# Performance work log

Measured on AMD Instinct MI355X. Metric: run time of the kernel, lower is better.

The kernel has to match this reference:

```python
import jax, jax.numpy as jnp
import numpy as np

NEG_INF = -1e9


def setup_inputs() -> dict:
    key = jax.random.key(0)
    ks = jax.random.split(key, 9)
    B, T, E, D, H = 64, 2048, 1024, 1024, 1024
    enc = jax.random.normal(ks[0], (B, T, E), dtype=jnp.float32)
    dec = jax.random.normal(ks[1], (B, D), dtype=jnp.float32)
    inp_mask = jax.random.randint(ks[2], (B, T), 0, 2, dtype=jnp.int32)
    s = 1.0 / np.sqrt(H)
    W_enc = jax.random.normal(ks[3], (E, H), dtype=jnp.float32) * s
    b_enc = jax.random.normal(ks[4], (H,), dtype=jnp.float32) * 0.01
    W_dec = jax.random.normal(ks[5], (D, H), dtype=jnp.float32) * s
    b_dec = jax.random.normal(ks[6], (H,), dtype=jnp.float32) * 0.01
    W_out = jax.random.normal(ks[7], (H, 1), dtype=jnp.float32) * s
    b_out = jax.random.normal(ks[8], (1,), dtype=jnp.float32) * 0.01
    return {"enc": enc, "dec": dec, "inp_mask": inp_mask,
            "W_enc": W_enc, "b_enc": b_enc, "W_dec": W_dec, "b_dec": b_dec,
            "W_out": W_out, "b_out": b_out}


def reference(enc, dec, inp_mask, W_enc, b_enc, W_dec, b_dec, W_out, b_out):
    # a: [B, T, H] = Linear(enc) + Linear(dec)[:, None, :]
    a = jnp.einsum('bte,eh->bth', enc, W_enc) + b_enc \
        + (dec @ W_dec + b_dec)[:, None, :]
    a = jnp.tanh(a)
    # scores: [B, T]
    scores = (jnp.einsum('bth,h->bt', a, W_out[:, 0]) + b_out[0])
    scores = jnp.where(inp_mask == 0, NEG_INF, scores)
    probs = jax.nn.softmax(scores, axis=1)            # [B, T]
    attn = jnp.einsum('bt,bte->be', probs, enc)       # [B, E]
    return (attn, probs)
```

## Files before the change

### kernel.cpp

```cpp
#include <hip/hip_runtime.h>
#include <hip/hip_bf16.h>

typedef __attribute__((ext_vector_type(4))) float f32x4;
typedef __attribute__((ext_vector_type(4))) unsigned int u32x4;

static constexpr int Bb = 64;
static constexpr int Tt = 2048;
static constexpr int Ee = 1024;
static constexpr int Hh = 1024;
static constexpr int ATTN_N = Bb * Ee;
static constexpr int PROB_N = Bb * Tt;

__device__ inline unsigned short f2bf(float f) {
    __hip_bfloat16 h = __float2bfloat16(f);
    return __builtin_bit_cast(unsigned short, h);
}

__device__ inline void gload_lds16(const unsigned short* g, unsigned short* l) {
    __builtin_amdgcn_global_load_lds(
        (const __attribute__((address_space(1))) void*)g,
        (__attribute__((address_space(3))) void*)l,
        16, 0, 0);
}

__global__ void wtrans_kernel(const float* __restrict__ w_enc,
                              unsigned short* __restrict__ w16t) {
    __shared__ float tile[32][33];
    const int bx = blockIdx.x & 31;
    const int by = blockIdx.x >> 5;
    const int tx = threadIdx.x & 31;
    const int ty = threadIdx.x >> 5;
#pragma unroll
    for (int j = 0; j < 4; ++j) {
        int e = by * 32 + ty + j * 8;
        int h = bx * 32 + tx;
        tile[ty + j * 8][tx] = w_enc[e * Hh + h];
    }
    __syncthreads();
#pragma unroll
    for (int j = 0; j < 4; ++j) {
        int h = bx * 32 + ty + j * 8;
        int e = by * 32 + tx;
        w16t[h * Ee + e] = f2bf(tile[tx][ty + j * 8]);
    }
}

__global__ void ddec_kernel(const float* __restrict__ dec,
                            const float* __restrict__ w_dec,
                            const float* __restrict__ b_dec,
                            const float* __restrict__ b_enc,
                            float* __restrict__ ddec) {
    const int b = blockIdx.y;
    const int h = blockIdx.x * 256 + threadIdx.x;
    float acc = b_dec[h] + b_enc[h];
    const float* dr = dec + b * Ee;
#pragma unroll 4
    for (int e = 0; e < Ee; ++e) {
        acc += dr[e] * w_dec[e * Hh + h];
    }
    ddec[b * Hh + h] = acc;
}

__global__ __launch_bounds__(512, 2) void gemm_score_kernel(
    const float* __restrict__ enc, const unsigned short* __restrict__ w16t,
    const float* __restrict__ ddec, const float* __restrict__ w_out,
    float* __restrict__ scores) {
    __shared__ unsigned short As[2][256 * 64];
    __shared__ unsigned short Bs[2][256 * 64];

    const int tid = threadIdx.x;
    const int lane = tid & 63;
    const int wid = tid >> 6;
    const int wm = wid >> 2;
    const int wn = wid & 3;
    const int lr = lane & 15;
    const int lg = lane >> 4;

    const int g = blockIdx.x;
    const int xcd = g & 7;
    const int slot = g >> 3;
    const int ntile = slot & 3;
    const int mtile = xcd * 64 + (slot >> 2);
    const int m0 = mtile * 256;
    const int n0 = ntile * 256;
    const int bidx = m0 >> 11;

    const int ar = tid >> 3;
    const int as = tid & 7;

    f32x4 aregs[8];

    auto loadA = [&](int kt) {
        const float* src = enc + (size_t)(m0 + ar) * Ee + kt * 64 + as * 8;
#pragma unroll
        for (int ci = 0; ci < 4; ++ci) {
            aregs[ci * 2]     = *reinterpret_cast<const f32x4*>(src + (size_t)(64 * ci) * Ee);
            aregs[ci * 2 + 1] = *reinterpret_cast<const f32x4*>(src + (size_t)(64 * ci) * Ee + 4);
        }
    };
    auto writeA = [&](int db) {
        char* abase = (char*)&As[db][0];
#pragma unroll
        for (int ci = 0; ci < 4; ++ci) {
            int r = ar + 64 * ci;
            u32x4 w;
            w.x = (unsigned)f2bf(aregs[2 * ci].x) | ((unsigned)f2bf(aregs[2 * ci].y) << 16);
            w.y = (unsigned)f2bf(aregs[2 * ci].z) | ((unsigned)f2bf(aregs[2 * ci].w) << 16);
            w.z = (unsigned)f2bf(aregs[2 * ci + 1].x) | ((unsigned)f2bf(aregs[2 * ci + 1].y) << 16);
            w.w = (unsigned)f2bf(aregs[2 * ci + 1].z) | ((unsigned)f2bf(aregs[2 * ci + 1].w) << 16);
            *reinterpret_cast<u32x4*>(abase + r * 128 + ((as * 16) ^ ((r & 7) << 4))) = w;
        }
    };
    auto stageB = [&](int kt, int db) {
        const int sg = (lane & 7) ^ (lane >> 3);
#pragma unroll
        for (int c = 0; c < 4; ++c) {
            int rr = (wid * 4 + c) * 8 + (lane >> 3);
            const unsigned short* src = w16t + (size_t)(n0 + rr) * Ee + kt * 64 + sg * 8;
            gload_lds16(src, &Bs[db][(wid * 4 + c) * 512]);
        }
    };

    f32x4 acc[8][4];
#pragma unroll
    for (int ni = 0; ni < 4; ++ni) {
        float dv = ddec[bidx * Hh + n0 + wn * 64 + ni * 16 + lr];
#pragma unroll
        for (int mi = 0; mi < 8; ++mi) {
            acc[mi][ni].x = dv; acc[mi][ni].y = dv;
            acc[mi][ni].z = dv; acc[mi][ni].w = dv;
        }
    }

    u32x4 af[4], bf[4];
    auto readB4 = [&](int db, int kh) {
        const char* bbase = (const char*)&Bs[db][0];
        const int kb = kh * 64 + lg * 16;
#pragma unroll
        for (int ni = 0; ni < 4; ++ni) {
            int r = wn * 64 + ni * 16 + lr;
            bf[ni] = *reinterpret_cast<const u32x4*>(bbase + r * 128 + (kb ^ ((r & 7) << 4)));
        }
    };
    auto readA4 = [&](int db, int kh, int mib) {
        const char* abase = (const char*)&As[db][0];
        const int kb = kh * 64 + lg * 16;
#pragma unroll
        for (int k = 0; k < 4; ++k) {
            int r = wm * 128 + (mib + k) * 16 + lr;
            af[k] = *reinterpret_cast<const u32x4*>(abase + r * 128 + (kb ^ ((r & 7) << 4)));
        }
    };
    auto mfma16 = [&](int mib) {
        __builtin_amdgcn_s_setprio(1);
#pragma unroll
        for (int k = 0; k < 4; ++k)
#pragma unroll
            for (int ni = 0; ni < 4; ++ni)
                asm("v_mfma_f32_16x16x32_bf16 %0, %1, %2, %0"
                    : "+v"(acc[mib + k][ni])
                    : "v"(af[k]), "v"(bf[ni]));
        __builtin_amdgcn_s_setprio(0);
    };

#define BARRIER() do { asm volatile("" ::: "memory"); \
    __builtin_amdgcn_s_barrier(); asm volatile("" ::: "memory"); } while (0)
#define LGKM0() asm volatile("s_waitcnt lgkmcnt(0)" ::: "memory")
#define VM0()   asm volatile("s_waitcnt vmcnt(0)" ::: "memory")

    loadA(0);
    stageB(0, 0);
    writeA(0);
    LGKM0();
    VM0();
    BARRIER();

#pragma unroll 1
    for (int t = 0; t < 16; ++t) {
        const int cur = t & 1;
        const bool stage = (t < 15);
        readB4(cur, 0);
        readA4(cur, 0, 0);
        if (stage) { stageB(t + 1, cur ^ 1); loadA(t + 1); }
        BARRIER(); LGKM0();
        mfma16(0);
        BARRIER();
        readA4(cur, 0, 4);
        BARRIER(); LGKM0();
        mfma16(4);
        BARRIER();
        readB4(cur, 1);
        readA4(cur, 1, 0);
        if (stage) writeA(cur ^ 1);
        BARRIER(); LGKM0();
        mfma16(0);
        BARRIER();
        readA4(cur, 1, 4);
        if (stage) VM0();
        BARRIER(); LGKM0();
        mfma16(4);
        BARRIER();
    }

    asm volatile("s_nop 7\n\ts_nop 7\n\ts_nop 7" ::: );

    float wout[4];
#pragma unroll
    for (int ni = 0; ni < 4; ++ni)
        wout[ni] = w_out[n0 + wn * 64 + ni * 16 + lr];

#pragma unroll
    for (int mi = 0; mi < 8; ++mi) {
#pragma unroll
        for (int i = 0; i < 4; ++i) {
            float s = 0.f;
#pragma unroll
            for (int ni = 0; ni < 4; ++ni) {
                float x = (i == 0) ? acc[mi][ni].x : (i == 1) ? acc[mi][ni].y
                           : (i == 2) ? acc[mi][ni].z : acc[mi][ni].w;
                float t = 1.f - 2.f / (__expf(2.f * x) + 1.f);
                s += t * wout[ni];
            }
            s += __shfl_xor(s, 1);
            s += __shfl_xor(s, 2);
            s += __shfl_xor(s, 4);
            s += __shfl_xor(s, 8);
            if (lr == 0) {
                int row = m0 + wm * 128 + mi * 16 + 4 * lg + i;
                atomicAdd(&scores[row], s);
            }
        }
    }
#undef BARRIER
#undef LGKM0
#undef VM0
}

__global__ __launch_bounds__(256) void softmax_kernel(float* __restrict__ sc,
                                                      const int* __restrict__ mask) {
    __shared__ float red[256];
    const int b = blockIdx.x;
    const int tid = threadIdx.x;
    float* row = sc + b * Tt;
    const int* mrow = mask + b * Tt;

    float v[8];
    float mx = -3.0e38f;
#pragma unroll
    for (int j = 0; j < 8; ++j) {
        int t = tid + j * 256;
        float s = row[t];
        v[j] = (mrow[t] == 0) ? -1.0e9f : s;
        mx = fmaxf(mx, v[j]);
    }
    red[tid] = mx;
    __syncthreads();
    for (int off = 128; off > 0; off >>= 1) {
        if (tid < off) red[tid] = fmaxf(red[tid], red[tid + off]);
        __syncthreads();
    }
    mx = red[0];
    __syncthreads();

    float p[8];
    float sum = 0.f;
#pragma unroll
    for (int j = 0; j < 8; ++j) {
        p[j] = __expf(v[j] - mx);
        sum += p[j];
    }
    red[tid] = sum;
    __syncthreads();
    for (int off = 128; off > 0; off >>= 1) {
        if (tid < off) red[tid] += red[tid + off];
        __syncthreads();
    }
    float inv = 1.f / red[0];
#pragma unroll
    for (int j = 0; j < 8; ++j)
        row[tid + j * 256] = p[j] * inv;
}

__global__ __launch_bounds__(256) void attn_kernel(const float* __restrict__ enc,
                                                   const float* __restrict__ probs,
                                                   float* __restrict__ attn) {
    __shared__ float pr[128];
    const int b = blockIdx.y;
    const int tc = blockIdx.x;
    const int tid = threadIdx.x;
    if (tid < 128) pr[tid] = probs[b * Tt + tc * 128 + tid];
    __syncthreads();

    const int e0 = tid * 4;
    f32x4 acc; acc.x = 0.f; acc.y = 0.f; acc.z = 0.f; acc.w = 0.f;
    const float* base = enc + (size_t)b * Tt * Ee + (size_t)tc * 128 * Ee + e0;
#pragma unroll 4
    for (int t = 0; t < 128; ++t) {
        f32x4 vv = *reinterpret_cast<const f32x4*>(base + (size_t)t * Ee);
        float pw = pr[t];
        acc.x += pw * vv.x; acc.y += pw * vv.y;
        acc.z += pw * vv.z; acc.w += pw * vv.w;
    }
    atomicAdd(&attn[b * Ee + e0 + 0], acc.x);
    atomicAdd(&attn[b * Ee + e0 + 1], acc.y);
    atomicAdd(&attn[b * Ee + e0 + 2], acc.z);
    atomicAdd(&attn[b * Ee + e0 + 3], acc.w);
}

extern "C" void kernel_launch(void* const* d_in, const int* in_sizes, int n_in,
                              void* d_out, int out_size, void* d_ws, size_t ws_size,
                              hipStream_t stream) {
    const float* enc      = (const float*)d_in[0];
    const float* dec      = (const float*)d_in[1];
    const int*   inp_mask = (const int*)d_in[2];
    const float* W_enc    = (const float*)d_in[3];
    const float* b_enc    = (const float*)d_in[4];
    const float* W_dec    = (const float*)d_in[5];
    const float* b_dec    = (const float*)d_in[6];
    const float* W_out    = (const float*)d_in[7];

    float* attn   = (float*)d_out;
    float* scores = (float*)d_out + ATTN_N;

    unsigned short* w16t = (unsigned short*)d_ws;
    float* ddec = attn;

    hipMemsetAsync(scores, 0, (size_t)PROB_N * sizeof(float), stream);

    wtrans_kernel<<<dim3(1024), 256, 0, stream>>>(W_enc, w16t);
    ddec_kernel<<<dim3(4, 64), 256, 0, stream>>>(dec, W_dec, b_dec, b_enc, ddec);
    gemm_score_kernel<<<dim3(2048), 512, 0, stream>>>(enc, w16t, ddec, W_out, scores);

    hipMemsetAsync(attn, 0, (size_t)ATTN_N * sizeof(float), stream);

    softmax_kernel<<<dim3(64), 256, 0, stream>>>(scores, inp_mask);
    attn_kernel<<<dim3(16, 64), 256, 0, stream>>>(enc, scores, attn);
}
```

Measured before the change: 665.4 us.

## Prefetch A tiles two k-steps ahead with double register buffers

The fp32 encoder A-tile global loads now go into two alternating register sets, so each load is issued two k-iterations before its LDS write instead of one. The main loop is unrolled by two so the register buffers can be swapped statically. Partial vmcnt waits replace the full drain, letting B staging finish while the next A loads stay in flight. This hides more global-memory latency at the cost of 32 extra VGPRs, which may reduce occupancy or cause spills.

```diff
diff --git a/kernel.cpp b/kernel.cpp
--- a/kernel.cpp
+++ b/kernel.cpp
@@ -88,26 +88,26 @@
     const int ar = tid >> 3;
     const int as = tid & 7;
 
-    f32x4 aregs[8];
-
-    auto loadA = [&](int kt) {
+    f32x4 rsA[8], rsB[8];
+
+    auto loadA = [&](int kt, f32x4 (&rs)[8]) {
         const float* src = enc + (size_t)(m0 + ar) * Ee + kt * 64 + as * 8;
 #pragma unroll
         for (int ci = 0; ci < 4; ++ci) {
-            aregs[ci * 2]     = *reinterpret_cast<const f32x4*>(src + (size_t)(64 * ci) * Ee);
-            aregs[ci * 2 + 1] = *reinterpret_cast<const f32x4*>(src + (size_t)(64 * ci) * Ee + 4);
-        }
-    };
-    auto writeA = [&](int db) {
+            rs[ci * 2]     = *reinterpret_cast<const f32x4*>(src + (size_t)(64 * ci) * Ee);
+            rs[ci * 2 + 1] = *reinterpret_cast<const f32x4*>(src + (size_t)(64 * ci) * Ee + 4);
+        }
+    };
+    auto writeA = [&](int db, f32x4 (&rs)[8]) {
         char* abase = (char*)&As[db][0];
 #pragma unroll
         for (int ci = 0; ci < 4; ++ci) {
             int r = ar + 64 * ci;
             u32x4 w;
-            w.x = (unsigned)f2bf(aregs[2 * ci].x) | ((unsigned)f2bf(aregs[2 * ci].y) << 16);
-            w.y = (unsigned)f2bf(aregs[2 * ci].z) | ((unsigned)f2bf(aregs[2 * ci].w) << 16);
-            w.z = (unsigned)f2bf(aregs[2 * ci + 1].x) | ((unsigned)f2bf(aregs[2 * ci + 1].y) << 16);
-            w.w = (unsigned)f2bf(aregs[2 * ci + 1].z) | ((unsigned)f2bf(aregs[2 * ci + 1].w) << 16);
+            w.x = (unsigned)f2bf(rs[2 * ci].x) | ((unsigned)f2bf(rs[2 * ci].y) << 16);
+            w.y = (unsigned)f2bf(rs[2 * ci].z) | ((unsigned)f2bf(rs[2 * ci].w) << 16);
+            w.z = (unsigned)f2bf(rs[2 * ci + 1].x) | ((unsigned)f2bf(rs[2 * ci + 1].y) << 16);
+            w.w = (unsigned)f2bf(rs[2 * ci + 1].z) | ((unsigned)f2bf(rs[2 * ci + 1].w) << 16);
             *reinterpret_cast<u32x4*>(abase + r * 128 + ((as * 16) ^ ((r & 7) << 4))) = w;
         }
     };
@@ -166,40 +166,49 @@
 #define BARRIER() do { asm volatile("" ::: "memory"); \
     __builtin_amdgcn_s_barrier(); asm volatile("" ::: "memory"); } while (0)
 #define LGKM0() asm volatile("s_waitcnt lgkmcnt(0)" ::: "memory")
-#define VM0()   asm volatile("s_waitcnt vmcnt(0)" ::: "memory")
-
-    loadA(0);
+
+    loadA(0, rsA);
     stageB(0, 0);
-    writeA(0);
+    writeA(0, rsA);
+    loadA(1, rsB);
+    asm volatile("s_waitcnt vmcnt(8)" ::: "memory");
     LGKM0();
-    VM0();
     BARRIER();
 
 #pragma unroll 1
-    for (int t = 0; t < 16; ++t) {
-        const int cur = t & 1;
-        const bool stage = (t < 15);
-        readB4(cur, 0);
-        readA4(cur, 0, 0);
-        if (stage) { stageB(t + 1, cur ^ 1); loadA(t + 1); }
-        BARRIER(); LGKM0();
-        mfma16(0);
-        BARRIER();
-        readA4(cur, 0, 4);
-        BARRIER(); LGKM0();
-        mfma16(4);
-        BARRIER();
-        readB4(cur, 1);
-        readA4(cur, 1, 0);
-        if (stage) writeA(cur ^ 1);
-        BARRIER(); LGKM0();
-        mfma16(0);
-        BARRIER();
-        readA4(cur, 1, 4);
-        if (stage) VM0();
-        BARRIER(); LGKM0();
-        mfma16(4);
-        BARRIER();
+    for (int tt = 0; tt < 16; tt += 2) {
+#pragma unroll
+        for (int p = 0; p < 2; ++p) {
+            const int t = tt + p;
+            f32x4 (&rs_next)[8] = (p == 0) ? rsA : rsB;
+            f32x4 (&rs_cur)[8]  = (p == 0) ? rsB : rsA;
+            readB4(p, 0);
+            readA4(p, 0, 0);
+            if (t < 15) stageB(t + 1, p ^ 1);
+            if (t < 14) loadA(t + 2, rs_next);
+            BARRIER(); LGKM0();
+            mfma16(0);
+            BARRIER();
+            readA4(p, 0, 4);
+            BARRIER(); LGKM0();
+            mfma16(4);
+            BARRIER();
+            readB4(p, 1);
+            readA4(p, 1, 0);
+            if (t < 15) writeA(p ^ 1, rs_cur);
+            BARRIER(); LGKM0();
+            mfma16(0);
+            BARRIER();
+            readA4(p, 1, 4);
+            if (t < 14) {
+                asm volatile("s_waitcnt vmcnt(8)" ::: "memory");
+            } else if (t == 14) {
+                asm volatile("s_waitcnt vmcnt(0)" ::: "memory");
+            }
+            BARRIER(); LGKM0();
+            mfma16(4);
+            BARRIER();
+        }
     }
 
     asm volatile("s_nop 7\n\ts_nop 7\n\ts_nop 7" ::: );
@@ -233,7 +242,6 @@
     }
 #undef BARRIER
 #undef LGKM0
-#undef VM0
 }
 
 __global__ __launch_bounds__(256) void softmax_kernel(float* __restrict__ sc,
```

Result: slower. 748.4 us (+12.5%).
